# Optimization experiments

Measured on AMD Instinct MI355X. Metric: run time of the kernel, lower is better.

## Reference

```python
import jax, jax.numpy as jnp
import numpy as np

S, B, C, H = 1024, 4, 1024, 16
CC = C // H


def setup_inputs() -> dict:
    key = jax.random.key(0)
    k0, k1, k2, k3, k4, k5 = jax.random.split(key, 6)
    x = jax.random.normal(k0, (S, B, C), jnp.float32)
    pe = jax.random.normal(k1, (S, B, C), jnp.float32)
    # causal content mask: True = masked (query i cannot attend key j > i)
    causal = np.triu(np.ones((S, S), dtype=bool), 1)
    content_mask = jnp.asarray(np.broadcast_to(causal[:, :, None], (S, S, B)))
    # per-batch tail padding; every sequence has >= 512 valid tokens
    lengths = np.array([S, S - 128, S - 256, S - 512])
    padding_mask = jnp.asarray(np.arange(S)[:, None] >= lengths[None, :])  # [s, b]
    sc = 1.0 / np.sqrt(C).astype(np.float32)
    Wqkv = jax.random.normal(k2, (3 * C, C), jnp.float32) * sc
    bqkv = jax.random.normal(k3, (3 * C,), jnp.float32) * 0.01
    Wo = jax.random.normal(k4, (C, C), jnp.float32) * sc
    bo = jax.random.normal(k5, (C,), jnp.float32) * 0.01
    return {"x": x, "pe": pe, "content_mask": content_mask,
            "padding_mask": padding_mask, "Wqkv": Wqkv, "bqkv": bqkv,
            "Wo": Wo, "bo": bo}


def reference(x, pe, content_mask, padding_mask, Wqkv, bqkv, Wo, bo):
    s, b, c = x.shape
    qkv = (x + pe) @ Wqkv.T + bqkv                       # [s, b, 3c]
    q, k, v = jnp.split(qkv, 3, axis=-1)
    q = q.reshape(s, b, H, CC)
    k = k.reshape(s, b, H, CC)
    v = v.reshape(s, b, H, CC)
    temperature = 1.0 / np.sqrt(CC).astype(np.float32)
    qk = jnp.einsum('sbhc,tbhc->stbh', q, k) * temperature  # [s, t, b, h]
    mask = content_mask[:, :, :, None] | padding_mask[None, :, :, None]
    a = jnp.where(mask, -jnp.inf, qk)
    p = jax.nn.softmax(a, axis=1)                        # softmax over key dim t
    out = jnp.einsum('stbh,tbhc->sbhc', p, v).reshape(s, b, c)
    return out @ Wo.T + bo
```

## Files before the change

### kernel.cpp

```cpp
#include <hip/hip_runtime.h>
#include <hip/hip_bf16.h>

#define S_  1024
#define B_  4
#define C_  1024
#define H_  16
#define CC_ 64
#define M_  (S_ * B_)
#define N_QKV (3 * C_)

typedef __bf16 bf16x8 __attribute__((ext_vector_type(8)));
typedef __bf16 bf16x4 __attribute__((ext_vector_type(4)));
typedef float  f32x4  __attribute__((ext_vector_type(4)));

__device__ __forceinline__ void gload16(const void* g, void* l) {
    __builtin_amdgcn_global_load_lds(
        (const __attribute__((address_space(1))) void*)g,
        (__attribute__((address_space(3))) void*)l, 16, 0, 0);
}

__global__ void prep_kernel(const float* __restrict__ x, const float* __restrict__ pe,
                            const float* __restrict__ Wqkv, const float* __restrict__ Wo,
                            __bf16* __restrict__ xpe, __bf16* __restrict__ wq,
                            __bf16* __restrict__ wo) {
    int bid = blockIdx.x;
    int t = threadIdx.x;
    if (bid < 4096) {
        int i = bid * 256 + t;
        float4 a = ((const float4*)x)[i];
        float4 p = ((const float4*)pe)[i];
        bf16x4 r;
        r[0] = (__bf16)(a.x + p.x); r[1] = (__bf16)(a.y + p.y);
        r[2] = (__bf16)(a.z + p.z); r[3] = (__bf16)(a.w + p.w);
        ((bf16x4*)xpe)[i] = r;
    } else if (bid < 7168) {
        int i = (bid - 4096) * 256 + t;
        float4 a = ((const float4*)Wqkv)[i];
        bf16x4 r;
        r[0] = (__bf16)a.x; r[1] = (__bf16)a.y; r[2] = (__bf16)a.z; r[3] = (__bf16)a.w;
        ((bf16x4*)wq)[i] = r;
    } else {
        int i = (bid - 7168) * 256 + t;
        float4 a = ((const float4*)Wo)[i];
        bf16x4 r;
        r[0] = (__bf16)a.x; r[1] = (__bf16)a.y; r[2] = (__bf16)a.z; r[3] = (__bf16)a.w;
        ((bf16x4*)wo)[i] = r;
    }
}

template<int EPI>
__global__ __launch_bounds__(256, 2)
void gemm_bt_kernel(const __bf16* __restrict__ A, const __bf16* __restrict__ B,
                    const float* __restrict__ bias, int M, int N, int K,
                    float* __restrict__ Cf, __bf16* __restrict__ Cq) {
    __shared__ __bf16 Als[128 * 32];
    __shared__ __bf16 Bls[128 * 32];

    const int tid  = threadIdx.x;
    const int lane = tid & 63;
    const int wid  = tid >> 6;
    const int quad = lane >> 4;
    const int l15  = lane & 15;
    const int wm   = wid >> 1;
    const int wn   = wid & 1;
    const int m0   = blockIdx.y * 128;
    const int n0   = blockIdx.x * 128;

    const int u0 = tid, u1 = 256 + tid;
    const int row0 = u0 >> 2, ch0 = (u0 & 3) * 8;
    const int row1 = u1 >> 2, ch1 = (u1 & 3) * 8;
    char* lA0 = (char*)Als + (size_t)(wid * 64) * 16;
    char* lA1 = (char*)Als + (size_t)(256 + wid * 64) * 16;
    char* lB0 = (char*)Bls + (size_t)(wid * 64) * 16;
    char* lB1 = (char*)Bls + (size_t)(256 + wid * 64) * 16;

    f32x4 acc[4][4];
#pragma unroll
    for (int i = 0; i < 4; i++)
#pragma unroll
        for (int j = 0; j < 4; j++) acc[i][j] = f32x4{0.f, 0.f, 0.f, 0.f};

    for (int k0 = 0; k0 < K; k0 += 32) {
        __syncthreads();
        gload16(&A[(size_t)(m0 + row0) * K + k0 + ch0], lA0);
        gload16(&A[(size_t)(m0 + row1) * K + k0 + ch1], lA1);
        gload16(&B[(size_t)(n0 + row0) * K + k0 + ch0], lB0);
        gload16(&B[(size_t)(n0 + row1) * K + k0 + ch1], lB1);
        __syncthreads();

        bf16x8 af[4], bfr[4];
#pragma unroll
        for (int mb = 0; mb < 4; mb++)
            af[mb] = *(const bf16x8*)&Als[(wm * 64 + mb * 16 + l15) * 32 + quad * 8];
#pragma unroll
        for (int nb = 0; nb < 4; nb++)
            bfr[nb] = *(const bf16x8*)&Bls[(wn * 64 + nb * 16 + l15) * 32 + quad * 8];

#pragma unroll
        for (int mb = 0; mb < 4; mb++)
#pragma unroll
            for (int nb = 0; nb < 4; nb++)
                acc[mb][nb] = __builtin_amdgcn_mfma_f32_16x16x32_bf16(
                    af[mb], bfr[nb], acc[mb][nb], 0, 0, 0);
    }

#pragma unroll
    for (int mb = 0; mb < 4; mb++) {
#pragma unroll
        for (int nb = 0; nb < 4; nb++) {
#pragma unroll
            for (int r = 0; r < 4; r++) {
                int m = m0 + wm * 64 + mb * 16 + quad * 4 + r;
                int n = n0 + wn * 64 + nb * 16 + l15;
                float v = acc[mb][nb][r] + bias[n];
                if (EPI == 0) {
                    Cf[(size_t)m * N + n] = v;
                } else {
                    int sec = n >> 10;
                    int c   = n & 1023;
                    int h   = c >> 6;
                    int cc  = c & 63;
                    int s   = m >> 2;
                    int b   = m & 3;
                    size_t off = ((((size_t)(sec * B_ + b) * H_ + h) * S_ + s) << 6) + cc;
                    Cq[off] = (__bf16)v;
                }
            }
        }
    }
}

__global__ __launch_bounds__(256, 4)
void vtrans_kernel(const __bf16* __restrict__ qkv, __bf16* __restrict__ vt) {
    __shared__ __bf16 T[64 * 68];
    const int s0 = blockIdx.x * 64;
    const int bh = blockIdx.y;
    const __bf16* vg = qkv + ((size_t)(2 * B_ * H_ + bh)) * S_ * CC_;
    __bf16* vo = vt + (size_t)bh * CC_ * S_;
    const int tid = threadIdx.x;
#pragma unroll
    for (int i = 0; i < 2; i++) {
        int u = i * 256 + tid;
        int r = u >> 3, c8 = (u & 7) * 8;
        bf16x8 v = *(const bf16x8*)&vg[(size_t)(s0 + r) * 64 + c8];
        bf16x4 lo, hi;
#pragma unroll
        for (int j = 0; j < 4; j++) { lo[j] = v[j]; hi[j] = v[j + 4]; }
        *(bf16x4*)&T[r * 68 + c8]     = lo;
        *(bf16x4*)&T[r * 68 + c8 + 4] = hi;
    }
    __syncthreads();
#pragma unroll
    for (int i = 0; i < 2; i++) {
        int u = i * 256 + tid;
        int cc = u >> 3, oc8 = (u & 7) * 8;
        bf16x8 o;
#pragma unroll
        for (int j = 0; j < 8; j++) o[j] = T[(oc8 + j) * 68 + cc];
        *(bf16x8*)&vo[(size_t)cc * S_ + s0 + oc8] = o;
    }
}

__global__ __launch_bounds__(256, 4)
void attn_kernel(const __bf16* __restrict__ qkv, const __bf16* __restrict__ vt,
                 __bf16* __restrict__ att) {
    const int qt  = 15 - blockIdx.x;
    const int bh  = blockIdx.y;
    const int b   = bh >> 4;
    const int h   = bh & 15;
    const int len = 1024 - ((b == 1) ? 128 : (b == 2) ? 256 : (b == 3) ? 512 : 0);

    const int tid  = threadIdx.x;
    const int w    = tid >> 6;
    const int lane = tid & 63;
    const int quad = lane >> 4;
    const int l15  = lane & 15;
    const int qbase = qt * 64;

    const size_t head  = ((size_t)(b * H_ + h)) * S_ * CC_;
    const size_t plane = (size_t)B_ * H_ * S_ * CC_;
    const __bf16* qg  = qkv + head;
    const __bf16* kg  = qkv + plane + head;
    const __bf16* vtg = vt + (size_t)bh * CC_ * S_;

    const int qw = qbase + w * 16;
    const int q  = qw + l15;
    bf16x8 qf0 = *(const bf16x8*)&qg[(size_t)q * 64 + quad * 8];
    bf16x8 qf1 = *(const bf16x8*)&qg[(size_t)q * 64 + 32 + quad * 8];

    __shared__ __bf16 Kls[64 * 72];
    __shared__ __bf16 Vtls[64 * 72];
    __shared__ __bf16 Pls[4 * 16 * 72];
    __bf16* pw = &Pls[w * 16 * 72];

    f32x4 oacc[4];
#pragma unroll
    for (int cb = 0; cb < 4; cb++) oacc[cb] = f32x4{0.f, 0.f, 0.f, 0.f};
    float m_i = -1e30f, l_i = 0.f;

    const int kend_blk = min(qbase + 64, len);
    const int kend_w   = min(qw + 16, len);
    const float temp = 0.125f;

    const int r0 = tid >> 3,          c0 = (tid & 7) * 8;
    const int r1 = (256 + tid) >> 3,  c1 = (tid & 7) * 8;

    for (int t0 = 0; t0 < kend_blk; t0 += 64) {
        __syncthreads();
        *(bf16x8*)&Kls[r0 * 72 + c0]  = *(const bf16x8*)&kg[(size_t)(t0 + r0) * 64 + c0];
        *(bf16x8*)&Kls[r1 * 72 + c1]  = *(const bf16x8*)&kg[(size_t)(t0 + r1) * 64 + c1];
        *(bf16x8*)&Vtls[r0 * 72 + c0] = *(const bf16x8*)&vtg[(size_t)r0 * S_ + t0 + c0];
        *(bf16x8*)&Vtls[r1 * 72 + c1] = *(const bf16x8*)&vtg[(size_t)r1 * S_ + t0 + c1];
        __syncthreads();
        if (t0 >= kend_w) continue;

        f32x4 sc[4];
#pragma unroll
        for (int nb = 0; nb < 4; nb++) {
            bf16x8 kf0 = *(const bf16x8*)&Kls[(nb * 16 + l15) * 72 + quad * 8];
            bf16x8 kf1 = *(const bf16x8*)&Kls[(nb * 16 + l15) * 72 + 32 + quad * 8];
            f32x4 s = f32x4{0.f, 0.f, 0.f, 0.f};
            s = __builtin_amdgcn_mfma_f32_16x16x32_bf16(kf0, qf0, s, 0, 0, 0);
            s = __builtin_amdgcn_mfma_f32_16x16x32_bf16(kf1, qf1, s, 0, 0, 0);
            sc[nb] = s;
        }
        if (t0 + 64 <= qw) {
#pragma unroll
            for (int nb = 0; nb < 4; nb++)
#pragma unroll
                for (int r = 0; r < 4; r++) sc[nb][r] *= temp;
        } else {
#pragma unroll
            for (int nb = 0; nb < 4; nb++) {
#pragma unroll
                for (int r = 0; r < 4; r++) {
                    int key = t0 + nb * 16 + quad * 4 + r;
                    float v = sc[nb][r] * temp;
                    sc[nb][r] = (key > q) ? -1e30f : v;
                }
            }
        }
        float mx0 = fmaxf(fmaxf(sc[0][0], sc[0][1]), fmaxf(sc[0][2], sc[0][3]));
        float mx1 = fmaxf(fmaxf(sc[1][0], sc[1][1]), fmaxf(sc[1][2], sc[1][3]));
        float mx2 = fmaxf(fmaxf(sc[2][0], sc[2][1]), fmaxf(sc[2][2], sc[2][3]));
        float mx3 = fmaxf(fmaxf(sc[3][0], sc[3][1]), fmaxf(sc[3][2], sc[3][3]));
        float mx = fmaxf(fmaxf(mx0, mx1), fmaxf(mx2, mx3));
        mx = fmaxf(mx, __shfl_xor(mx, 16, 64));
        mx = fmaxf(mx, __shfl_xor(mx, 32, 64));
        float m_new = fmaxf(m_i, mx);
        float alpha = __expf(m_i - m_new);
        m_i = m_new;
        float sum = 0.f;
#pragma unroll
        for (int nb = 0; nb < 4; nb++) {
#pragma unroll
            for (int r = 0; r < 4; r++) {
                float pv = __expf(sc[nb][r] - m_new);
                sc[nb][r] = pv;
                sum += pv;
            }
        }
        sum += __shfl_xor(sum, 16, 64);
        sum += __shfl_xor(sum, 32, 64);
        l_i = l_i * alpha + sum;
#pragma unroll
        for (int cb = 0; cb < 4; cb++)
#pragma unroll
            for (int r = 0; r < 4; r++) oacc[cb][r] *= alpha;

#pragma unroll
        for (int nb = 0; nb < 4; nb++) {
            bf16x4 pk;
#pragma unroll
            for (int r = 0; r < 4; r++) pk[r] = (__bf16)sc[nb][r];
            *(bf16x4*)&pw[l15 * 72 + nb * 16 + quad * 4] = pk;
        }
        asm volatile("s_waitcnt lgkmcnt(0)" ::: "memory");
        bf16x8 pf0 = *(const bf16x8*)&pw[l15 * 72 + quad * 8];
        bf16x8 pf1 = *(const bf16x8*)&pw[l15 * 72 + 32 + quad * 8];

#pragma unroll
        for (int cb = 0; cb < 4; cb++) {
            bf16x8 vf0 = *(const bf16x8*)&Vtls[(cb * 16 + l15) * 72 + quad * 8];
            bf16x8 vf1 = *(const bf16x8*)&Vtls[(cb * 16 + l15) * 72 + 32 + quad * 8];
            oacc[cb] = __builtin_amdgcn_mfma_f32_16x16x32_bf16(vf0, pf0, oacc[cb], 0, 0, 0);
            oacc[cb] = __builtin_amdgcn_mfma_f32_16x16x32_bf16(vf1, pf1, oacc[cb], 0, 0, 0);
        }
    }

    float inv = 1.f / l_i;
    size_t rowoff = ((size_t)(q * B_ + b)) * C_ + h * 64;
#pragma unroll
    for (int cb = 0; cb < 4; cb++) {
        bf16x4 ov;
#pragma unroll
        for (int r = 0; r < 4; r++) ov[r] = (__bf16)(oacc[cb][r] * inv);
        *(bf16x4*)&att[rowoff + cb * 16 + quad * 4] = ov;
    }
}

extern "C" void kernel_launch(void* const* d_in, const int* in_sizes, int n_in,
                              void* d_out, int out_size, void* d_ws, size_t ws_size,
                              hipStream_t stream) {
    const float* x     = (const float*)d_in[0];
    const float* pe    = (const float*)d_in[1];
    const float* Wqkv  = (const float*)d_in[4];
    const float* bqkv  = (const float*)d_in[5];
    const float* Wo    = (const float*)d_in[6];
    const float* bo    = (const float*)d_in[7];
    float* out = (float*)d_out;

    __bf16* xpe   = (__bf16*)d_ws;
    __bf16* wqkvb = xpe + (size_t)M_ * C_;
    __bf16* wob   = wqkvb + (size_t)N_QKV * C_;
    __bf16* qkvb  = wob + (size_t)C_ * C_;
    __bf16* attb  = qkvb + (size_t)3 * B_ * H_ * S_ * CC_;
    __bf16* vtb   = attb + (size_t)M_ * C_;

    prep_kernel<<<8192, 256, 0, stream>>>(x, pe, Wqkv, Wo, xpe, wqkvb, wob);

    gemm_bt_kernel<1><<<dim3(N_QKV / 128, M_ / 128), 256, 0, stream>>>(
        xpe, wqkvb, bqkv, M_, N_QKV, C_, nullptr, qkvb);

    vtrans_kernel<<<dim3(S_ / 64, B_ * H_), 256, 0, stream>>>(qkvb, vtb);

    attn_kernel<<<dim3(S_ / 64, B_ * H_), 256, 0, stream>>>(qkvb, vtb, attb);

    gemm_bt_kernel<0><<<dim3(C_ / 128, M_ / 128), 256, 0, stream>>>(
        attb, wob, bo, M_, C_, C_, out, nullptr);
}
```

Before: 201.4 us.

## Double-buffer K/V tiles in attention and use narrower N tile for output GEMM

The attention kernel now double-buffers K and V^T tiles in shared memory. It prefetches the next tile into registers while computing the current one, which removes one barrier per iteration and hides global-load latency. The output projection GEMM is templated on the N tile width and launched with 64-wide tiles, doubling the block count from 256 to 512 to fill the CUs better. The costs are more shared memory and registers in attention (launch bounds lowered from 4 to 3 blocks) and less reuse of A per block in the output GEMM.

```diff
diff --git a/kernel.cpp b/kernel.cpp
--- a/kernel.cpp
+++ b/kernel.cpp
@@ -48,13 +48,14 @@
     }
 }
 
-template<int EPI>
+template<int EPI, int BN>
 __global__ __launch_bounds__(256, 2)
 void gemm_bt_kernel(const __bf16* __restrict__ A, const __bf16* __restrict__ B,
                     const float* __restrict__ bias, int M, int N, int K,
                     float* __restrict__ Cf, __bf16* __restrict__ Cq) {
+    constexpr int NB = BN / 32;
     __shared__ __bf16 Als[128 * 32];
-    __shared__ __bf16 Bls[128 * 32];
+    __shared__ __bf16 Bls[BN * 32];
 
     const int tid  = threadIdx.x;
     const int lane = tid & 63;
@@ -64,7 +65,7 @@
     const int wm   = wid >> 1;
     const int wn   = wid & 1;
     const int m0   = blockIdx.y * 128;
-    const int n0   = blockIdx.x * 128;
+    const int n0   = blockIdx.x * BN;
 
     const int u0 = tid, u1 = 256 + tid;
     const int row0 = u0 >> 2, ch0 = (u0 & 3) * 8;
@@ -74,32 +75,33 @@
     char* lB0 = (char*)Bls + (size_t)(wid * 64) * 16;
     char* lB1 = (char*)Bls + (size_t)(256 + wid * 64) * 16;
 
-    f32x4 acc[4][4];
+    f32x4 acc[4][NB];
 #pragma unroll
     for (int i = 0; i < 4; i++)
 #pragma unroll
-        for (int j = 0; j < 4; j++) acc[i][j] = f32x4{0.f, 0.f, 0.f, 0.f};
+        for (int j = 0; j < NB; j++) acc[i][j] = f32x4{0.f, 0.f, 0.f, 0.f};
 
     for (int k0 = 0; k0 < K; k0 += 32) {
         __syncthreads();
         gload16(&A[(size_t)(m0 + row0) * K + k0 + ch0], lA0);
         gload16(&A[(size_t)(m0 + row1) * K + k0 + ch1], lA1);
         gload16(&B[(size_t)(n0 + row0) * K + k0 + ch0], lB0);
-        gload16(&B[(size_t)(n0 + row1) * K + k0 + ch1], lB1);
+        if (BN == 128)
+            gload16(&B[(size_t)(n0 + row1) * K + k0 + ch1], lB1);
         __syncthreads();
 
-        bf16x8 af[4], bfr[4];
+        bf16x8 af[4], bfr[NB];
 #pragma unroll
         for (int mb = 0; mb < 4; mb++)
             af[mb] = *(const bf16x8*)&Als[(wm * 64 + mb * 16 + l15) * 32 + quad * 8];
 #pragma unroll
-        for (int nb = 0; nb < 4; nb++)
-            bfr[nb] = *(const bf16x8*)&Bls[(wn * 64 + nb * 16 + l15) * 32 + quad * 8];
+        for (int nb = 0; nb < NB; nb++)
+            bfr[nb] = *(const bf16x8*)&Bls[(wn * (BN / 2) + nb * 16 + l15) * 32 + quad * 8];
 
 #pragma unroll
         for (int mb = 0; mb < 4; mb++)
 #pragma unroll
-            for (int nb = 0; nb < 4; nb++)
+            for (int nb = 0; nb < NB; nb++)
                 acc[mb][nb] = __builtin_amdgcn_mfma_f32_16x16x32_bf16(
                     af[mb], bfr[nb], acc[mb][nb], 0, 0, 0);
     }
@@ -107,11 +109,11 @@
 #pragma unroll
     for (int mb = 0; mb < 4; mb++) {
 #pragma unroll
-        for (int nb = 0; nb < 4; nb++) {
+        for (int nb = 0; nb < NB; nb++) {
 #pragma unroll
             for (int r = 0; r < 4; r++) {
                 int m = m0 + wm * 64 + mb * 16 + quad * 4 + r;
-                int n = n0 + wn * 64 + nb * 16 + l15;
+                int n = n0 + wn * (BN / 2) + nb * 16 + l15;
                 float v = acc[mb][nb][r] + bias[n];
                 if (EPI == 0) {
                     Cf[(size_t)m * N + n] = v;
@@ -161,7 +163,7 @@
     }
 }
 
-__global__ __launch_bounds__(256, 4)
+__global__ __launch_bounds__(256, 3)
 void attn_kernel(const __bf16* __restrict__ qkv, const __bf16* __restrict__ vt,
                  __bf16* __restrict__ att) {
     const int qt  = 15 - blockIdx.x;
@@ -188,8 +190,8 @@
     bf16x8 qf0 = *(const bf16x8*)&qg[(size_t)q * 64 + quad * 8];
     bf16x8 qf1 = *(const bf16x8*)&qg[(size_t)q * 64 + 32 + quad * 8];
 
-    __shared__ __bf16 Kls[64 * 72];
-    __shared__ __bf16 Vtls[64 * 72];
+    __shared__ __bf16 Kls[2][64 * 72];
+    __shared__ __bf16 Vtls[2][64 * 72];
     __shared__ __bf16 Pls[4 * 16 * 72];
     __bf16* pw = &Pls[w * 16 * 72];
 
@@ -205,87 +207,111 @@
     const int r0 = tid >> 3,          c0 = (tid & 7) * 8;
     const int r1 = (256 + tid) >> 3,  c1 = (tid & 7) * 8;
 
+    *(bf16x8*)&Kls[0][r0 * 72 + c0]  = *(const bf16x8*)&kg[(size_t)r0 * 64 + c0];
+    *(bf16x8*)&Kls[0][r1 * 72 + c1]  = *(const bf16x8*)&kg[(size_t)r1 * 64 + c1];
+    *(bf16x8*)&Vtls[0][r0 * 72 + c0] = *(const bf16x8*)&vtg[(size_t)r0 * S_ + c0];
+    *(bf16x8*)&Vtls[0][r1 * 72 + c1] = *(const bf16x8*)&vtg[(size_t)r1 * S_ + c1];
+    __syncthreads();
+
     for (int t0 = 0; t0 < kend_blk; t0 += 64) {
+        const int cur = (t0 >> 6) & 1;
+        const bool has_next = (t0 + 64) < kend_blk;
+
+        bf16x8 nk0, nk1, nv0, nv1;
+        if (has_next) {
+            const int t1 = t0 + 64;
+            nk0 = *(const bf16x8*)&kg[(size_t)(t1 + r0) * 64 + c0];
+            nk1 = *(const bf16x8*)&kg[(size_t)(t1 + r1) * 64 + c1];
+            nv0 = *(const bf16x8*)&vtg[(size_t)r0 * S_ + t1 + c0];
+            nv1 = *(const bf16x8*)&vtg[(size_t)r1 * S_ + t1 + c1];
+        }
+
+        if (t0 < kend_w) {
+            const __bf16* Kb  = Kls[cur];
+            const __bf16* Vb  = Vtls[cur];
+
+            f32x4 sc[4];
+#pragma unroll
+            for (int nb = 0; nb < 4; nb++) {
+                bf16x8 kf0 = *(const bf16x8*)&Kb[(nb * 16 + l15) * 72 + quad * 8];
+                bf16x8 kf1 = *(const bf16x8*)&Kb[(nb * 16 + l15) * 72 + 32 + quad * 8];
+                f32x4 s = f32x4{0.f, 0.f, 0.f, 0.f};
+                s = __builtin_amdgcn_mfma_f32_16x16x32_bf16(kf0, qf0, s, 0, 0, 0);
+                s = __builtin_amdgcn_mfma_f32_16x16x32_bf16(kf1, qf1, s, 0, 0, 0);
+                sc[nb] = s;
+            }
+            if (t0 + 64 <= qw) {
+#pragma unroll
+                for (int nb = 0; nb < 4; nb++)
+#pragma unroll
+                    for (int r = 0; r < 4; r++) sc[nb][r] *= temp;
+            } else {
+#pragma unroll
+                for (int nb = 0; nb < 4; nb++) {
+#pragma unroll
+                    for (int r = 0; r < 4; r++) {
+                        int key = t0 + nb * 16 + quad * 4 + r;
+                        float v = sc[nb][r] * temp;
+                        sc[nb][r] = (key > q) ? -1e30f : v;
+                    }
+                }
+            }
+            float mx0 = fmaxf(fmaxf(sc[0][0], sc[0][1]), fmaxf(sc[0][2], sc[0][3]));
+            float mx1 = fmaxf(fmaxf(sc[1][0], sc[1][1]), fmaxf(sc[1][2], sc[1][3]));
+            float mx2 = fmaxf(fmaxf(sc[2][0], sc[2][1]), fmaxf(sc[2][2], sc[2][3]));
+            float mx3 = fmaxf(fmaxf(sc[3][0], sc[3][1]), fmaxf(sc[3][2], sc[3][3]));
+            float mx = fmaxf(fmaxf(mx0, mx1), fmaxf(mx2, mx3));
+            mx = fmaxf(mx, __shfl_xor(mx, 16, 64));
+            mx = fmaxf(mx, __shfl_xor(mx, 32, 64));
+            float m_new = fmaxf(m_i, mx);
+            float alpha = __expf(m_i - m_new);
+            m_i = m_new;
+            float sum = 0.f;
+#pragma unroll
+            for (int nb = 0; nb < 4; nb++) {
+#pragma unroll
+                for (int r = 0; r < 4; r++) {
+                    float pv = __expf(sc[nb][r] - m_new);
+                    sc[nb][r] = pv;
+                    sum += pv;
+                }
+            }
+            sum += __shfl_xor(sum, 16, 64);
+            sum += __shfl_xor(sum, 32, 64);
+            l_i = l_i * alpha + sum;
+#pragma unroll
+            for (int cb = 0; cb < 4; cb++)
+#pragma unroll
+                for (int r = 0; r < 4; r++) oacc[cb][r] *= alpha;
+
+#pragma unroll
+            for (int nb = 0; nb < 4; nb++) {
+                bf16x4 pk;
+#pragma unroll
+                for (int r = 0; r < 4; r++) pk[r] = (__bf16)sc[nb][r];
+                *(bf16x4*)&pw[l15 * 72 + nb * 16 + quad * 4] = pk;
+            }
+            asm volatile("s_waitcnt lgkmcnt(0)" ::: "memory");
+            bf16x8 pf0 = *(const bf16x8*)&pw[l15 * 72 + quad * 8];
+            bf16x8 pf1 = *(const bf16x8*)&pw[l15 * 72 + 32 + quad * 8];
+
+#pragma unroll
+            for (int cb = 0; cb < 4; cb++) {
+                bf16x8 vf0 = *(const bf16x8*)&Vb[(cb * 16 + l15) * 72 + quad * 8];
+                bf16x8 vf1 = *(const bf16x8*)&Vb[(cb * 16 + l15) * 72 + 32 + quad * 8];
+                oacc[cb] = __builtin_amdgcn_mfma_f32_16x16x32_bf16(vf0, pf0, oacc[cb], 0, 0, 0);
+                oacc[cb] = __builtin_amdgcn_mfma_f32_16x16x32_bf16(vf1, pf1, oacc[cb], 0, 0, 0);
+            }
+        }
+
+        if (has_next) {
+            const int nb_ = cur ^ 1;
+            *(bf16x8*)&Kls[nb_][r0 * 72 + c0]  = nk0;
+            *(bf16x8*)&Kls[nb_][r1 * 72 + c1]  = nk1;
+            *(bf16x8*)&Vtls[nb_][r0 * 72 + c0] = nv0;
+            *(bf16x8*)&Vtls[nb_][r1 * 72 + c1] = nv1;
+        }
         __syncthreads();
-        *(bf16x8*)&Kls[r0 * 72 + c0]  = *(const bf16x8*)&kg[(size_t)(t0 + r0) * 64 + c0];
-        *(bf16x8*)&Kls[r1 * 72 + c1]  = *(const bf16x8*)&kg[(size_t)(t0 + r1) * 64 + c1];
-        *(bf16x8*)&Vtls[r0 * 72 + c0] = *(const bf16x8*)&vtg[(size_t)r0 * S_ + t0 + c0];
-        *(bf16x8*)&Vtls[r1 * 72 + c1] = *(const bf16x8*)&vtg[(size_t)r1 * S_ + t0 + c1];
-        __syncthreads();
-        if (t0 >= kend_w) continue;
-
-        f32x4 sc[4];
-#pragma unroll
-        for (int nb = 0; nb < 4; nb++) {
-            bf16x8 kf0 = *(const bf16x8*)&Kls[(nb * 16 + l15) * 72 + quad * 8];
-            bf16x8 kf1 = *(const bf16x8*)&Kls[(nb * 16 + l15) * 72 + 32 + quad * 8];
-            f32x4 s = f32x4{0.f, 0.f, 0.f, 0.f};
-            s = __builtin_amdgcn_mfma_f32_16x16x32_bf16(kf0, qf0, s, 0, 0, 0);
-            s = __builtin_amdgcn_mfma_f32_16x16x32_bf16(kf1, qf1, s, 0, 0, 0);
-            sc[nb] = s;
-        }
-        if (t0 + 64 <= qw) {
-#pragma unroll
-            for (int nb = 0; nb < 4; nb++)
-#pragma unroll
-                for (int r = 0; r < 4; r++) sc[nb][r] *= temp;
-        } else {
-#pragma unroll
-            for (int nb = 0; nb < 4; nb++) {
-#pragma unroll
-                for (int r = 0; r < 4; r++) {
-                    int key = t0 + nb * 16 + quad * 4 + r;
-                    float v = sc[nb][r] * temp;
-                    sc[nb][r] = (key > q) ? -1e30f : v;
-                }
-            }
-        }
-        float mx0 = fmaxf(fmaxf(sc[0][0], sc[0][1]), fmaxf(sc[0][2], sc[0][3]));
-        float mx1 = fmaxf(fmaxf(sc[1][0], sc[1][1]), fmaxf(sc[1][2], sc[1][3]));
-        float mx2 = fmaxf(fmaxf(sc[2][0], sc[2][1]), fmaxf(sc[2][2], sc[2][3]));
-        float mx3 = fmaxf(fmaxf(sc[3][0], sc[3][1]), fmaxf(sc[3][2], sc[3][3]));
-        float mx = fmaxf(fmaxf(mx0, mx1), fmaxf(mx2, mx3));
-        mx = fmaxf(mx, __shfl_xor(mx, 16, 64));
-        mx = fmaxf(mx, __shfl_xor(mx, 32, 64));
-        float m_new = fmaxf(m_i, mx);
-        float alpha = __expf(m_i - m_new);
-        m_i = m_new;
-        float sum = 0.f;
-#pragma unroll
-        for (int nb = 0; nb < 4; nb++) {
-#pragma unroll
-            for (int r = 0; r < 4; r++) {
-                float pv = __expf(sc[nb][r] - m_new);
-                sc[nb][r] = pv;
-                sum += pv;
-            }
-        }
-        sum += __shfl_xor(sum, 16, 64);
-        sum += __shfl_xor(sum, 32, 64);
-        l_i = l_i * alpha + sum;
-#pragma unroll
-        for (int cb = 0; cb < 4; cb++)
-#pragma unroll
-            for (int r = 0; r < 4; r++) oacc[cb][r] *= alpha;
-
-#pragma unroll
-        for (int nb = 0; nb < 4; nb++) {
-            bf16x4 pk;
-#pragma unroll
-            for (int r = 0; r < 4; r++) pk[r] = (__bf16)sc[nb][r];
-            *(bf16x4*)&pw[l15 * 72 + nb * 16 + quad * 4] = pk;
-        }
-        asm volatile("s_waitcnt lgkmcnt(0)" ::: "memory");
-        bf16x8 pf0 = *(const bf16x8*)&pw[l15 * 72 + quad * 8];
-        bf16x8 pf1 = *(const bf16x8*)&pw[l15 * 72 + 32 + quad * 8];
-
-#pragma unroll
-        for (int cb = 0; cb < 4; cb++) {
-            bf16x8 vf0 = *(const bf16x8*)&Vtls[(cb * 16 + l15) * 72 + quad * 8];
-            bf16x8 vf1 = *(const bf16x8*)&Vtls[(cb * 16 + l15) * 72 + 32 + quad * 8];
-            oacc[cb] = __builtin_amdgcn_mfma_f32_16x16x32_bf16(vf0, pf0, oacc[cb], 0, 0, 0);
-            oacc[cb] = __builtin_amdgcn_mfma_f32_16x16x32_bf16(vf1, pf1, oacc[cb], 0, 0, 0);
-        }
     }
 
     float inv = 1.f / l_i;
@@ -319,13 +345,13 @@
 
     prep_kernel<<<8192, 256, 0, stream>>>(x, pe, Wqkv, Wo, xpe, wqkvb, wob);
 
-    gemm_bt_kernel<1><<<dim3(N_QKV / 128, M_ / 128), 256, 0, stream>>>(
+    gemm_bt_kernel<1, 128><<<dim3(N_QKV / 128, M_ / 128), 256, 0, stream>>>(
         xpe, wqkvb, bqkv, M_, N_QKV, C_, nullptr, qkvb);
 
     vtrans_kernel<<<dim3(S_ / 64, B_ * H_), 256, 0, stream>>>(qkvb, vtb);
 
     attn_kernel<<<dim3(S_ / 64, B_ * H_), 256, 0, stream>>>(qkvb, vtb, attb);
 
-    gemm_bt_kernel<0><<<dim3(C_ / 128, M_ / 128), 256, 0, stream>>>(
+    gemm_bt_kernel<0, 64><<<dim3(C_ / 64, M_ / 128), 256, 0, stream>>>(
         attb, wob, bo, M_, C_, C_, out, nullptr);
 }
```

Measured after the change: 205.7 us. +2.1%, slower.
